# Kernel optimization log

Hardware: AMD Instinct MI355X
Metric: run time of the kernel (lower is better)

## Reference

```python
import jax, jax.numpy as jnp
import numpy as np

B, C, H, W = 2, 64, 192, 192
K = 3
KK = K * K  # 9 kernel taps


def conv2d(x, w, b, dilation=1, padding=1):
    # NCHW / OIHW 3x3 conv, stride 1
    out = jax.lax.conv_general_dilated(
        x, w, window_strides=(1, 1),
        padding=[(padding, padding), (padding, padding)],
        rhs_dilation=(dilation, dilation),
        dimension_numbers=('NCHW', 'OIHW', 'NCHW'))
    return out + b[None, :, None, None]


def channel_ln(x, w, b, eps=1e-5):
    # WithBias_LayerNorm over the channel axis (to_3d puts C last)
    mu = jnp.mean(x, axis=1, keepdims=True)
    var = jnp.mean((x - mu) ** 2, axis=1, keepdims=True)  # biased var
    xn = (x - mu) / jnp.sqrt(var + eps)
    return xn * w[None, :, None, None] + b[None, :, None, None]


def mod_deform_conv(x, offset, mask, w, b):
    # Modulated deformable conv (mmcv semantics): stride 1, pad 1, dil 1,
    # deform_groups=1. offset: [B,2*KK,H,W] (dy,dx interleaved per tap),
    # mask: [B,KK,H,W].
    Bb, Cc, Hh, Ww = x.shape
    off = offset.reshape(Bb, KK, 2, Hh, Ww)
    kidx = jnp.arange(K)
    ky, kx = jnp.meshgrid(kidx, kidx, indexing='ij')
    ky = ky.reshape(KK).astype(x.dtype)
    kx = kx.reshape(KK).astype(x.dtype)
    hh = jnp.arange(Hh, dtype=x.dtype)
    ww = jnp.arange(Ww, dtype=x.dtype)
    # sample positions: out_pos - pad + tap + learned offset  -> [B,KK,H,W]
    py = off[:, :, 0] + hh[None, None, :, None] - 1.0 + ky[None, :, None, None]
    px = off[:, :, 1] + ww[None, None, None, :] - 1.0 + kx[None, :, None, None]
    y0f = jnp.floor(py)
    x0f = jnp.floor(px)
    ly = py - y0f
    lx = px - x0f
    y0 = y0f.astype(jnp.int32)
    x0 = x0f.astype(jnp.int32)
    xf = x.reshape(Bb, Cc, Hh * Ww)

    def corner(yi, xi, wgt):
        valid = (yi >= 0) & (yi < Hh) & (xi >= 0) & (xi < Ww)
        idx = (jnp.clip(yi, 0, Hh - 1) * Ww + jnp.clip(xi, 0, Ww - 1)).reshape(Bb, -1)
        g = jax.vmap(lambda xb, ib: xb[:, ib])(xf, idx)  # [B,C,KK*H*W]
        wv = (wgt * valid.astype(x.dtype)).reshape(Bb, 1, -1)
        return g * wv

    val = (corner(y0, x0, (1 - ly) * (1 - lx))
           + corner(y0, x0 + 1, (1 - ly) * lx)
           + corner(y0 + 1, x0, ly * (1 - lx))
           + corner(y0 + 1, x0 + 1, ly * lx))
    val = val.reshape(Bb, Cc, KK, Hh, Ww) * mask[:, None]  # modulate
    out = jnp.einsum('bckhw,ock->bohw', val, w.reshape(w.shape[0], Cc, KK))
    return out + b[None, :, None, None]


def setup_inputs() -> dict:
    key = jax.random.key(0)
    ks = jax.random.split(key, 8)
    x = jax.random.normal(ks[0], (B, C, H, W), jnp.float32)
    pre_mask = jax.random.uniform(ks[1], (B, 1, H, W), jnp.float32)
    ln_w = jnp.ones((C,), jnp.float32)
    ln_b = jnp.zeros((C,), jnp.float32)
    # offset/mask convs are zero-init in the original; use small random
    # weights so the bilinear gather is actually exercised (offsets ~ few px)
    off_w = jax.random.normal(ks[2], (2 * KK, C, 3, 3), jnp.float32) * 0.02
    off_b = jnp.zeros((2 * KK,), jnp.float32)
    mask_w = jax.random.normal(ks[3], (KK, C, 3, 3), jnp.float32) * 0.02
    mask_b = jnp.zeros((KK,), jnp.float32)
    scale = 1.0 / np.sqrt(C * KK)
    def_w = jax.random.normal(ks[4], (C, C, 3, 3), jnp.float32) * scale
    def_b = jnp.zeros((C,), jnp.float32)
    fus_w = jax.random.normal(ks[5], (C, C, 3, 3), jnp.float32) * scale
    fus_b = jnp.zeros((C,), jnp.float32)
    return {'x': x, 'pre_mask': pre_mask, 'ln_w': ln_w, 'ln_b': ln_b,
            'off_w': off_w, 'off_b': off_b, 'mask_w': mask_w, 'mask_b': mask_b,
            'def_w': def_w, 'def_b': def_b, 'fus_w': fus_w, 'fus_b': fus_b}


def reference(x, pre_mask, ln_w, ln_b, off_w, off_b, mask_w, mask_b,
              def_w, def_b, fus_w, fus_b):
    inp = x
    xn = channel_ln(x, ln_w, ln_b)
    # only the dilation=1 offset/mask branch feeds the single def_conv
    offset = conv2d(xn, off_w, off_b, dilation=1, padding=1)
    mask = jax.nn.sigmoid(conv2d(xn, mask_w, mask_b, dilation=1, padding=1))
    x_def = mod_deform_conv(xn, offset, mask, def_w, def_b)
    # single def_conv -> stack+sum is identity
    return conv2d(x_def, fus_w, fus_b) * pre_mask + inp * (1.0 - pre_mask)
```

## Files before the change

### kernel.cpp

```cpp
#include <hip/hip_runtime.h>
#include <hip/hip_bf16.h>
#include <math.h>

#define B_ 2
#define C_ 64
#define H_ 192
#define W_ 192
#define HW_ (H_*W_)
#define BHW_ (B_*HW_)
#define KK_ 9
#define CK_ (C_*KK_)
#define KSTEPS_ (CK_/32)
#define TX_ 12
#define WROWS_ 8
#define WCOLS_ 21
#define WCHUNKS_ (WROWS_*WCOLS_*8)
#define FWROWS_ 6
#define FWCOLS_ 18
#define FWCHUNKS_ (FWROWS_*FWCOLS_*8)

typedef __bf16 bf16x8 __attribute__((ext_vector_type(8)));
typedef float  f32x4  __attribute__((ext_vector_type(4)));
typedef unsigned short ushortx8 __attribute__((ext_vector_type(8)));
typedef unsigned short ushortx4 __attribute__((ext_vector_type(4)));

__device__ __forceinline__ float bf2f(unsigned short u) {
    unsigned int t = ((unsigned int)u) << 16;
    return __builtin_bit_cast(float, t);
}
__device__ __forceinline__ unsigned short f2bf(float f) {
    __hip_bfloat16 hb = __float2bfloat16(f);
    return *reinterpret_cast<unsigned short*>(&hb);
}

__global__ void ln_kernel(const float* __restrict__ x,
                          const float* __restrict__ lnw,
                          const float* __restrict__ lnb,
                          unsigned short* __restrict__ xnb) {
    int p = blockIdx.x * blockDim.x + threadIdx.x;
    if (p >= BHW_) return;
    int b = p / HW_, pix = p % HW_;
    const float* xb = x + (size_t)b * C_ * HW_ + pix;
    float v[C_];
    float s = 0.f, s2 = 0.f;
    #pragma unroll
    for (int c = 0; c < C_; ++c) {
        v[c] = xb[(size_t)c * HW_];
        s += v[c]; s2 += v[c] * v[c];
    }
    float mu  = s * (1.0f / C_);
    float var = s2 * (1.0f / C_) - mu * mu;
    float inv = rsqrtf(var + 1e-5f);
    unsigned short* zb = xnb + (size_t)p * 64;
    #pragma unroll
    for (int g = 0; g < 8; ++g) {
        ushortx8 st;
        #pragma unroll
        for (int j = 0; j < 8; ++j) {
            int c = g * 8 + j;
            st[j] = f2bf((v[c] - mu) * inv * lnw[c] + lnb[c]);
        }
        *reinterpret_cast<ushortx8*>(zb + g * 8) = st;
    }
}

__global__ void prepack_kernel(const float* __restrict__ dw,
                               const float* __restrict__ fw,
                               const float* __restrict__ offw,
                               const float* __restrict__ maskw,
                               unsigned short* __restrict__ wpack,
                               unsigned short* __restrict__ wpf,
                               unsigned short* __restrict__ wpc) {
    const int n1 = 4 * KSTEPS_ * 64 * 8;
    const int n2 = 4 * KSTEPS_ * 64 * 8;
    const int n3 = 2 * KSTEPS_ * 64 * 8;
    int gid = blockIdx.x * blockDim.x + threadIdx.x;
    int nth = gridDim.x * blockDim.x;
    for (int idx = gid; idx < n1 + n2 + n3; idx += nth) {
        int which = (idx < n1) ? 0 : (idx < n1 + n2 ? 1 : 2);
        int rem = idx - (which == 0 ? 0 : (which == 1 ? n1 : n1 + n2));
        int j = rem & 7;
        int l = (rem >> 3) & 63;
        int rest = rem >> 9;
        int s = rest % KSTEPS_;
        int t = rest / KSTEPS_;
        int oc = t * 16 + (l & 15);
        int ck = s * 32 + (l >> 4) * 8 + j;
        int k = ck >> 6, c = ck & 63;
        float v;
        if (which == 0) {
            v = dw[(size_t)oc * CK_ + c * 9 + k];
        } else if (which == 1) {
            v = fw[(size_t)oc * CK_ + c * 9 + k];
        } else {
            v = (oc < 18) ? offw[(size_t)oc * CK_ + c * 9 + k]
              : (oc < 27) ? maskw[(size_t)(oc - 18) * CK_ + c * 9 + k]
              : 0.f;
        }
        unsigned short u = f2bf(v);
        if (which == 0) wpack[rem] = u;
        else if (which == 1) wpf[rem] = u;
        else wpc[rem] = u;
    }
}

__global__ void __launch_bounds__(128) dc_mfma(
        const unsigned short* __restrict__ xnb,
        const unsigned short* __restrict__ wpc,
        const float* __restrict__ offb, const float* __restrict__ maskb,
        const unsigned short* __restrict__ wpack,
        const float* __restrict__ db,
        unsigned short* __restrict__ xdefb) {
    __shared__ ushortx8 win[WCHUNKS_];
    __shared__ float som[2][32][36];
    int tid  = threadIdx.x;
    int wave = tid >> 6;
    int lane = tid & 63;
    int bid  = blockIdx.x;
    int rg   = bid % (H_ / 4);
    int rest = bid / (H_ / 4);
    int tx   = rest % TX_;
    int b    = rest / TX_;
    int pq = lane & 15;
    int kchunk = lane >> 4;
    int h0 = rg * 4;
    int w0 = tx * 16, w = w0 + pq;
    int hh0 = h0 + 2 * wave, hh1 = hh0 + 1;

    const unsigned short* xb = xnb + (size_t)b * HW_ * 64;

    #pragma unroll
    for (int i = 0; i < 11; ++i) {
        int idx = i * 128 + tid;
        if (idx < WCHUNKS_) {
            int r    = idx / (WCOLS_ * 8);
            int rem2 = idx - r * (WCOLS_ * 8);
            int c    = rem2 >> 3;
            int seg  = rem2 & 7;
            int gy = min(max(h0 - 2 + r, 0), H_ - 1);
            int gx = min(max(w0 - 2 + c, 0), W_ - 1);
            ushortx8 v = *reinterpret_cast<const ushortx8*>(
                xb + ((size_t)(gy * W_ + gx) * 64 + seg * 8));
            win[(r * WCOLS_ + c) * 8 + (seg ^ (c & 7))] = v;
        }
    }
    __syncthreads();

    f32x4 cacc[2][2];
    #pragma unroll
    for (int pg = 0; pg < 2; ++pg)
        #pragma unroll
        for (int t = 0; t < 2; ++t) cacc[pg][t] = f32x4{0.f, 0.f, 0.f, 0.f};

    #pragma unroll
    for (int s = 0; s < KSTEPS_; ++s) {
        const int k = s >> 1;
        const int dy = k / 3 - 1, dxk = k % 3 - 1;
        int wc = pq + dxk + 2;
        int sidx = ((s & 1) * 4 + kchunk) ^ (wc & 7);
        bf16x8 bv[2];
        #pragma unroll
        for (int pg = 0; pg < 2; ++pg) {
            int hp = (pg ? hh1 : hh0);
            bool ok = ((unsigned)(hp + dy) < (unsigned)H_) &&
                      ((unsigned)(w + dxk) < (unsigned)W_);
            int wr = 2 * wave + pg + dy + 2;
            ushortx8 u = win[(wr * WCOLS_ + wc) * 8 + sidx];
            if (!ok) u = ushortx8{0, 0, 0, 0, 0, 0, 0, 0};
            bv[pg] = __builtin_bit_cast(bf16x8, u);
        }
        #pragma unroll
        for (int t = 0; t < 2; ++t) {
            bf16x8 afrag = *reinterpret_cast<const bf16x8*>(
                wpc + ((size_t)(t * KSTEPS_ + s) * 64 + lane) * 8);
            cacc[0][t] = __builtin_amdgcn_mfma_f32_16x16x32_bf16(afrag, bv[0], cacc[0][t], 0, 0, 0);
            cacc[1][t] = __builtin_amdgcn_mfma_f32_16x16x32_bf16(afrag, bv[1], cacc[1][t], 0, 0, 0);
        }
    }

    #pragma unroll
    for (int pg = 0; pg < 2; ++pg) {
        #pragma unroll
        for (int t = 0; t < 2; ++t) {
            f32x4 sv;
            #pragma unroll
            for (int r = 0; r < 4; ++r) {
                int oc = t * 16 + kchunk * 4 + r;
                float a = cacc[pg][t][r];
                if (oc < 18)      sv[r] = a + offb[oc];
                else if (oc < 27) sv[r] = 1.f / (1.f + expf(-(a + maskb[oc - 18])));
                else              sv[r] = 0.f;
            }
            *reinterpret_cast<f32x4*>(&som[wave][pg * 16 + pq][t * 16 + kchunk * 4]) = sv;
        }
    }

    const float* omA = som[wave][pq];
    const float* omB = som[wave][16 + pq];

    f32x4 acc[2][4];
    #pragma unroll
    for (int pg = 0; pg < 2; ++pg)
        #pragma unroll
        for (int t = 0; t < 4; ++t) acc[pg][t] = f32x4{0.f, 0.f, 0.f, 0.f};

    #pragma unroll
    for (int k = 0; k < KK_; ++k) {
        float qA[4], qB[4];
        int cbA[4], sxA[4], cbB[4], sxB[4];
        bool inA[4], inB[4];
        int gaA[4], gaB[4];
        #pragma unroll
        for (int pg = 0; pg < 2; ++pg) {
            const float* om = pg ? omB : omA;
            int hp = pg ? hh1 : hh0;
            float dy = om[2 * k], dx = om[2 * k + 1], m = om[18 + k];
            float py = dy + (float)(hp - 1 + k / 3);
            float px = dx + (float)(w - 1 + k % 3);
            float fy = floorf(py), fx = floorf(px);
            float ly = py - fy, lx = px - fx;
            int y0 = (int)fy, x0 = (int)fx;
            int y1 = y0 + 1, x1 = x0 + 1;
            bool oky0 = (unsigned)y0 < (unsigned)H_;
            bool oky1 = (unsigned)y1 < (unsigned)H_;
            bool okx0 = (unsigned)x0 < (unsigned)W_;
            bool okx1 = (unsigned)x1 < (unsigned)W_;
            float* q = pg ? qB : qA;
            q[0] = (oky0 && okx0) ? (1.f - ly) * (1.f - lx) * m : 0.f;
            q[1] = (oky0 && okx1) ? (1.f - ly) * lx * m : 0.f;
            q[2] = (oky1 && okx0) ? ly * (1.f - lx) * m : 0.f;
            q[3] = (oky1 && okx1) ? ly * lx * m : 0.f;
            int wr0 = y0 - (h0 - 2), wr1 = y1 - (h0 - 2);
            int wc0 = x0 - (w0 - 2), wc1 = x1 - (w0 - 2);
            bool inr0 = (unsigned)wr0 < (unsigned)WROWS_;
            bool inr1 = (unsigned)wr1 < (unsigned)WROWS_;
            bool inc0 = (unsigned)wc0 < (unsigned)WCOLS_;
            bool inc1 = (unsigned)wc1 < (unsigned)WCOLS_;
            bool* in = pg ? inB : inA;
            in[0] = inr0 && inc0; in[1] = inr0 && inc1;
            in[2] = inr1 && inc0; in[3] = inr1 && inc1;
            int swr0 = min(max(wr0, 0), WROWS_ - 1), swr1 = min(max(wr1, 0), WROWS_ - 1);
            int swc0 = min(max(wc0, 0), WCOLS_ - 1), swc1 = min(max(wc1, 0), WCOLS_ - 1);
            int* cb = pg ? cbB : cbA;
            int* sx = pg ? sxB : sxA;
            cb[0] = (swr0 * WCOLS_ + swc0) * 8; sx[0] = swc0 & 7;
            cb[1] = (swr0 * WCOLS_ + swc1) * 8; sx[1] = swc1 & 7;
            cb[2] = (swr1 * WCOLS_ + swc0) * 8; sx[2] = swc0 & 7;
            cb[3] = (swr1 * WCOLS_ + swc1) * 8; sx[3] = swc1 & 7;
            int cy0 = min(max(y0, 0), H_ - 1), cy1 = min(max(y1, 0), H_ - 1);
            int cx0 = min(max(x0, 0), W_ - 1), cx1 = min(max(x1, 0), W_ - 1);
            int* ga = pg ? gaB : gaA;
            ga[0] = cy0 * W_ + cx0; ga[1] = cy0 * W_ + cx1;
            ga[2] = cy1 * W_ + cx0; ga[3] = cy1 * W_ + cx1;
        }

        #pragma unroll
        for (int half = 0; half < 2; ++half) {
            int s = k * 2 + half;
            int seg = half * 4 + kchunk;
            int cbg = half * 32 + kchunk * 8;
            bf16x8 af[4];
            #pragma unroll
            for (int t = 0; t < 4; ++t)
                af[t] = *reinterpret_cast<const bf16x8*>(
                    wpack + ((size_t)(t * KSTEPS_ + s) * 64 + lane) * 8);
            ushortx8 vA[4], vB[4];
            #pragma unroll
            for (int c = 0; c < 4; ++c) vA[c] = win[cbA[c] + (seg ^ sxA[c])];
            #pragma unroll
            for (int c = 0; c < 4; ++c) vB[c] = win[cbB[c] + (seg ^ sxB[c])];
            #pragma unroll
            for (int c = 0; c < 4; ++c) {
                if (qA[c] != 0.f && !inA[c])
                    vA[c] = *reinterpret_cast<const ushortx8*>(xb + ((size_t)gaA[c] * 64 + cbg));
                if (qB[c] != 0.f && !inB[c])
                    vB[c] = *reinterpret_cast<const ushortx8*>(xb + ((size_t)gaB[c] * 64 + cbg));
            }
            union { unsigned short u[8]; bf16x8 v; } buA, buB;
            #pragma unroll
            for (int j = 0; j < 8; ++j) {
                float a = qA[0] * bf2f(vA[0][j]) + qA[1] * bf2f(vA[1][j])
                        + qA[2] * bf2f(vA[2][j]) + qA[3] * bf2f(vA[3][j]);
                buA.u[j] = f2bf(a);
                float bvv = qB[0] * bf2f(vB[0][j]) + qB[1] * bf2f(vB[1][j])
                          + qB[2] * bf2f(vB[2][j]) + qB[3] * bf2f(vB[3][j]);
                buB.u[j] = f2bf(bvv);
            }
            #pragma unroll
            for (int t = 0; t < 4; ++t) {
                acc[0][t] = __builtin_amdgcn_mfma_f32_16x16x32_bf16(af[t], buA.v, acc[0][t], 0, 0, 0);
                acc[1][t] = __builtin_amdgcn_mfma_f32_16x16x32_bf16(af[t], buB.v, acc[1][t], 0, 0, 0);
            }
        }
    }

    #pragma unroll
    for (int pg = 0; pg < 2; ++pg) {
        int hp = pg ? hh1 : hh0;
        unsigned short* zb = xdefb + ((size_t)(b * HW_ + hp * W_ + w)) * 64;
        #pragma unroll
        for (int t = 0; t < 4; ++t) {
            ushortx4 st;
            #pragma unroll
            for (int r = 0; r < 4; ++r) {
                int oc = t * 16 + kchunk * 4 + r;
                st[r] = f2bf(acc[pg][t][r] + db[oc]);
            }
            *reinterpret_cast<ushortx4*>(zb + t * 16 + kchunk * 4) = st;
        }
    }
}

__global__ void __launch_bounds__(128) fuse_mfma(
        const unsigned short* __restrict__ xdefb,
        const unsigned short* __restrict__ wpf,
        const float* __restrict__ fb,
        const float* __restrict__ premask,
        const float* __restrict__ xin,
        float* __restrict__ out) {
    __shared__ ushortx8 fwin[FWCHUNKS_];
    int tid  = threadIdx.x;
    int wave = tid >> 6;
    int lane = tid & 63;
    int bid  = blockIdx.x;
    int rg   = bid % (H_ / 4);
    int rest = bid / (H_ / 4);
    int tx   = rest % TX_;
    int b    = rest / TX_;
    int pq = lane & 15;
    int kchunk = lane >> 4;
    int h0 = rg * 4;
    int w0 = tx * 16, w = w0 + pq;
    int hh0 = h0 + 2 * wave, hh1 = hh0 + 1;

    const unsigned short* xb = xdefb + (size_t)b * HW_ * 64;

    #pragma unroll
    for (int i = 0; i < 7; ++i) {
        int idx = i * 128 + tid;
        if (idx < FWCHUNKS_) {
            int r    = idx / (FWCOLS_ * 8);
            int rem2 = idx - r * (FWCOLS_ * 8);
            int c    = rem2 >> 3;
            int seg  = rem2 & 7;
            int gy = min(max(h0 - 1 + r, 0), H_ - 1);
            int gx = min(max(w0 - 1 + c, 0), W_ - 1);
            ushortx8 v = *reinterpret_cast<const ushortx8*>(
                xb + ((size_t)(gy * W_ + gx) * 64 + seg * 8));
            fwin[(r * FWCOLS_ + c) * 8 + (seg ^ (c & 7))] = v;
        }
    }
    __syncthreads();

    f32x4 acc[2][4];
    #pragma unroll
    for (int pg = 0; pg < 2; ++pg)
        #pragma unroll
        for (int t = 0; t < 4; ++t) acc[pg][t] = f32x4{0.f, 0.f, 0.f, 0.f};

    #pragma unroll
    for (int s = 0; s < KSTEPS_; ++s) {
        const int k = s >> 1;
        const int dy = k / 3 - 1, dxk = k % 3 - 1;
        int wc = pq + dxk + 1;
        int sidx = ((s & 1) * 4 + kchunk) ^ (wc & 7);
        bf16x8 bv[2];
        #pragma unroll
        for (int pg = 0; pg < 2; ++pg) {
            int hp = (pg ? hh1 : hh0);
            bool ok = ((unsigned)(hp + dy) < (unsigned)H_) &&
                      ((unsigned)(w + dxk) < (unsigned)W_);
            int wr = 2 * wave + pg + dy + 1;
            ushortx8 u = fwin[(wr * FWCOLS_ + wc) * 8 + sidx];
            if (!ok) u = ushortx8{0, 0, 0, 0, 0, 0, 0, 0};
            bv[pg] = __builtin_bit_cast(bf16x8, u);
        }
        #pragma unroll
        for (int t = 0; t < 4; ++t) {
            bf16x8 afrag = *reinterpret_cast<const bf16x8*>(
                wpf + ((size_t)(t * KSTEPS_ + s) * 64 + lane) * 8);
            acc[0][t] = __builtin_amdgcn_mfma_f32_16x16x32_bf16(afrag, bv[0], acc[0][t], 0, 0, 0);
            acc[1][t] = __builtin_amdgcn_mfma_f32_16x16x32_bf16(afrag, bv[1], acc[1][t], 0, 0, 0);
        }
    }

    #pragma unroll
    for (int pg = 0; pg < 2; ++pg) {
        int hp = pg ? hh1 : hh0;
        int pix = hp * W_ + w;
        float pm = premask[(size_t)b * HW_ + pix];
        #pragma unroll
        for (int t = 0; t < 4; ++t) {
            #pragma unroll
            for (int r = 0; r < 4; ++r) {
                int oc = t * 16 + kchunk * 4 + r;
                size_t oidx = ((size_t)b * C_ + oc) * HW_ + pix;
                out[oidx] = (acc[pg][t][r] + fb[oc]) * pm + xin[oidx] * (1.f - pm);
            }
        }
    }
}

extern "C" void kernel_launch(void* const* d_in, const int* in_sizes, int n_in,
                              void* d_out, int out_size, void* d_ws, size_t ws_size,
                              hipStream_t stream) {
    const float* x       = (const float*)d_in[0];
    const float* premask = (const float*)d_in[1];
    const float* lnw     = (const float*)d_in[2];
    const float* lnb     = (const float*)d_in[3];
    const float* offw    = (const float*)d_in[4];
    const float* offb    = (const float*)d_in[5];
    const float* maskw   = (const float*)d_in[6];
    const float* maskb   = (const float*)d_in[7];
    const float* dw      = (const float*)d_in[8];
    const float* db      = (const float*)d_in[9];
    const float* fw      = (const float*)d_in[10];
    const float* fb      = (const float*)d_in[11];
    float* out = (float*)d_out;

    char* ws = (char*)d_ws;
    unsigned short* xnb   = (unsigned short*)ws;  ws += sizeof(short) * (size_t)BHW_ * 64;
    unsigned short* xdefb = (unsigned short*)ws;  ws += sizeof(short) * (size_t)BHW_ * 64;
    unsigned short* wpack = (unsigned short*)ws;  ws += sizeof(short) * 4 * KSTEPS_ * 64 * 8;
    unsigned short* wpf   = (unsigned short*)ws;  ws += sizeof(short) * 4 * KSTEPS_ * 64 * 8;
    unsigned short* wpc   = (unsigned short*)ws;  ws += sizeof(short) * 2 * KSTEPS_ * 64 * 8;

    const int grid = B_ * TX_ * (H_ / 4);

    ln_kernel<<<(BHW_ + 255) / 256, 256, 0, stream>>>(x, lnw, lnb, xnb);
    prepack_kernel<<<36, 256, 0, stream>>>(dw, fw, offw, maskw, wpack, wpf, wpc);
    dc_mfma<<<grid, 128, 0, stream>>>(
        xnb, wpc, offb, maskb, wpack, db, xdefb);
    fuse_mfma<<<grid, 128, 0, stream>>>(xdefb, wpf, fb, premask, x, out);
}
```

Before: 79.00 us.

## Process four rows per wave and merge LayerNorm with weight prepacking

Each block now covers 8 output rows instead of 4, so each wave handles 4 rows. Loaded weight fragments are reused across four pixel groups, and the halo overhead of the shared-memory window shrinks relative to the tile. The LayerNorm and weight-prepack kernels are merged into one launch that selects its work by block index, removing one launch. The trade-off is a larger accumulator register footprint and half as many blocks (576), which may lower occupancy and fill the GPU less evenly.

After: 94.25 us. 19.3% more time.

```diff
diff --git a/kernel.cpp b/kernel.cpp
--- a/kernel.cpp
+++ b/kernel.cpp
@@ -12,10 +12,11 @@
 #define CK_ (C_*KK_)
 #define KSTEPS_ (CK_/32)
 #define TX_ 12
-#define WROWS_ 8
+#define RB_ 8
+#define WROWS_ 12
 #define WCOLS_ 21
 #define WCHUNKS_ (WROWS_*WCOLS_*8)
-#define FWROWS_ 6
+#define FWROWS_ 10
 #define FWCOLS_ 18
 #define FWCHUNKS_ (FWROWS_*FWCOLS_*8)
 
@@ -33,49 +34,49 @@
     return *reinterpret_cast<unsigned short*>(&hb);
 }
 
-__global__ void ln_kernel(const float* __restrict__ x,
-                          const float* __restrict__ lnw,
-                          const float* __restrict__ lnb,
-                          unsigned short* __restrict__ xnb) {
-    int p = blockIdx.x * blockDim.x + threadIdx.x;
-    if (p >= BHW_) return;
-    int b = p / HW_, pix = p % HW_;
-    const float* xb = x + (size_t)b * C_ * HW_ + pix;
-    float v[C_];
-    float s = 0.f, s2 = 0.f;
-    #pragma unroll
-    for (int c = 0; c < C_; ++c) {
-        v[c] = xb[(size_t)c * HW_];
-        s += v[c]; s2 += v[c] * v[c];
-    }
-    float mu  = s * (1.0f / C_);
-    float var = s2 * (1.0f / C_) - mu * mu;
-    float inv = rsqrtf(var + 1e-5f);
-    unsigned short* zb = xnb + (size_t)p * 64;
-    #pragma unroll
-    for (int g = 0; g < 8; ++g) {
-        ushortx8 st;
-        #pragma unroll
-        for (int j = 0; j < 8; ++j) {
-            int c = g * 8 + j;
-            st[j] = f2bf((v[c] - mu) * inv * lnw[c] + lnb[c]);
-        }
-        *reinterpret_cast<ushortx8*>(zb + g * 8) = st;
-    }
-}
-
-__global__ void prepack_kernel(const float* __restrict__ dw,
-                               const float* __restrict__ fw,
-                               const float* __restrict__ offw,
-                               const float* __restrict__ maskw,
-                               unsigned short* __restrict__ wpack,
-                               unsigned short* __restrict__ wpf,
-                               unsigned short* __restrict__ wpc) {
+__global__ void ln_prepack_kernel(const float* __restrict__ x,
+                                  const float* __restrict__ lnw,
+                                  const float* __restrict__ lnb,
+                                  unsigned short* __restrict__ xnb,
+                                  const float* __restrict__ dw,
+                                  const float* __restrict__ fw,
+                                  const float* __restrict__ offw,
+                                  const float* __restrict__ maskw,
+                                  unsigned short* __restrict__ wpack,
+                                  unsigned short* __restrict__ wpf,
+                                  unsigned short* __restrict__ wpc) {
+    if (blockIdx.x < 288) {
+        int p = blockIdx.x * 256 + threadIdx.x;
+        int b = p / HW_, pix = p % HW_;
+        const float* xb = x + (size_t)b * C_ * HW_ + pix;
+        float v[C_];
+        float s = 0.f, s2 = 0.f;
+        #pragma unroll
+        for (int c = 0; c < C_; ++c) {
+            v[c] = xb[(size_t)c * HW_];
+            s += v[c]; s2 += v[c] * v[c];
+        }
+        float mu  = s * (1.0f / C_);
+        float var = s2 * (1.0f / C_) - mu * mu;
+        float inv = rsqrtf(var + 1e-5f);
+        unsigned short* zb = xnb + (size_t)p * 64;
+        #pragma unroll
+        for (int g = 0; g < 8; ++g) {
+            ushortx8 st;
+            #pragma unroll
+            for (int j = 0; j < 8; ++j) {
+                int c = g * 8 + j;
+                st[j] = f2bf((v[c] - mu) * inv * lnw[c] + lnb[c]);
+            }
+            *reinterpret_cast<ushortx8*>(zb + g * 8) = st;
+        }
+        return;
+    }
     const int n1 = 4 * KSTEPS_ * 64 * 8;
     const int n2 = 4 * KSTEPS_ * 64 * 8;
     const int n3 = 2 * KSTEPS_ * 64 * 8;
-    int gid = blockIdx.x * blockDim.x + threadIdx.x;
-    int nth = gridDim.x * blockDim.x;
+    int gid = (blockIdx.x - 288) * 256 + threadIdx.x;
+    int nth = 36 * 256;
     for (int idx = gid; idx < n1 + n2 + n3; idx += nth) {
         int which = (idx < n1) ? 0 : (idx < n1 + n2 ? 1 : 2);
         int rem = idx - (which == 0 ? 0 : (which == 1 ? n1 : n1 + n2));
@@ -112,25 +113,25 @@
         const float* __restrict__ db,
         unsigned short* __restrict__ xdefb) {
     __shared__ ushortx8 win[WCHUNKS_];
-    __shared__ float som[2][32][36];
+    __shared__ float som[2][64][36];
     int tid  = threadIdx.x;
     int wave = tid >> 6;
     int lane = tid & 63;
     int bid  = blockIdx.x;
-    int rg   = bid % (H_ / 4);
-    int rest = bid / (H_ / 4);
+    int rg   = bid % (H_ / RB_);
+    int rest = bid / (H_ / RB_);
     int tx   = rest % TX_;
     int b    = rest / TX_;
     int pq = lane & 15;
     int kchunk = lane >> 4;
-    int h0 = rg * 4;
+    int h0 = rg * RB_;
     int w0 = tx * 16, w = w0 + pq;
-    int hh0 = h0 + 2 * wave, hh1 = hh0 + 1;
+    int hbase = h0 + 4 * wave;
 
     const unsigned short* xb = xnb + (size_t)b * HW_ * 64;
 
     #pragma unroll
-    for (int i = 0; i < 11; ++i) {
+    for (int i = 0; i < 16; ++i) {
         int idx = i * 128 + tid;
         if (idx < WCHUNKS_) {
             int r    = idx / (WCOLS_ * 8);
@@ -146,9 +147,9 @@
     }
     __syncthreads();
 
-    f32x4 cacc[2][2];
-    #pragma unroll
-    for (int pg = 0; pg < 2; ++pg)
+    f32x4 cacc[4][2];
+    #pragma unroll
+    for (int pg = 0; pg < 4; ++pg)
         #pragma unroll
         for (int t = 0; t < 2; ++t) cacc[pg][t] = f32x4{0.f, 0.f, 0.f, 0.f};
 
@@ -158,28 +159,28 @@
         const int dy = k / 3 - 1, dxk = k % 3 - 1;
         int wc = pq + dxk + 2;
         int sidx = ((s & 1) * 4 + kchunk) ^ (wc & 7);
-        bf16x8 bv[2];
-        #pragma unroll
-        for (int pg = 0; pg < 2; ++pg) {
-            int hp = (pg ? hh1 : hh0);
+        bf16x8 af[2];
+        #pragma unroll
+        for (int t = 0; t < 2; ++t)
+            af[t] = *reinterpret_cast<const bf16x8*>(
+                wpc + ((size_t)(t * KSTEPS_ + s) * 64 + lane) * 8);
+        #pragma unroll
+        for (int pg = 0; pg < 4; ++pg) {
+            int hp = hbase + pg;
             bool ok = ((unsigned)(hp + dy) < (unsigned)H_) &&
                       ((unsigned)(w + dxk) < (unsigned)W_);
-            int wr = 2 * wave + pg + dy + 2;
+            int wr = 4 * wave + pg + dy + 2;
             ushortx8 u = win[(wr * WCOLS_ + wc) * 8 + sidx];
             if (!ok) u = ushortx8{0, 0, 0, 0, 0, 0, 0, 0};
-            bv[pg] = __builtin_bit_cast(bf16x8, u);
-        }
-        #pragma unroll
-        for (int t = 0; t < 2; ++t) {
-            bf16x8 afrag = *reinterpret_cast<const bf16x8*>(
-                wpc + ((size_t)(t * KSTEPS_ + s) * 64 + lane) * 8);
-            cacc[0][t] = __builtin_amdgcn_mfma_f32_16x16x32_bf16(afrag, bv[0], cacc[0][t], 0, 0, 0);
-            cacc[1][t] = __builtin_amdgcn_mfma_f32_16x16x32_bf16(afrag, bv[1], cacc[1][t], 0, 0, 0);
-        }
-    }
-
-    #pragma unroll
-    for (int pg = 0; pg < 2; ++pg) {
+            bf16x8 bv = __builtin_bit_cast(bf16x8, u);
+            #pragma unroll
+            for (int t = 0; t < 2; ++t)
+                cacc[pg][t] = __builtin_amdgcn_mfma_f32_16x16x32_bf16(af[t], bv, cacc[pg][t], 0, 0, 0);
+        }
+    }
+
+    #pragma unroll
+    for (int pg = 0; pg < 4; ++pg) {
         #pragma unroll
         for (int t = 0; t < 2; ++t) {
             f32x4 sv;
@@ -195,25 +196,26 @@
         }
     }
 
-    const float* omA = som[wave][pq];
-    const float* omB = som[wave][16 + pq];
-
-    f32x4 acc[2][4];
-    #pragma unroll
-    for (int pg = 0; pg < 2; ++pg)
+    f32x4 acc[4][4];
+    #pragma unroll
+    for (int pg = 0; pg < 4; ++pg)
         #pragma unroll
         for (int t = 0; t < 4; ++t) acc[pg][t] = f32x4{0.f, 0.f, 0.f, 0.f};
 
     #pragma unroll
     for (int k = 0; k < KK_; ++k) {
-        float qA[4], qB[4];
-        int cbA[4], sxA[4], cbB[4], sxB[4];
-        bool inA[4], inB[4];
-        int gaA[4], gaB[4];
-        #pragma unroll
-        for (int pg = 0; pg < 2; ++pg) {
-            const float* om = pg ? omB : omA;
-            int hp = pg ? hh1 : hh0;
+        bf16x8 af[2][4];
+        #pragma unroll
+        for (int half = 0; half < 2; ++half)
+            #pragma unroll
+            for (int t = 0; t < 4; ++t)
+                af[half][t] = *reinterpret_cast<const bf16x8*>(
+                    wpack + ((size_t)(t * KSTEPS_ + (k * 2 + half)) * 64 + lane) * 8);
+
+        #pragma unroll
+        for (int pg = 0; pg < 4; ++pg) {
+            int hp = hbase + pg;
+            const float* om = som[wave][pg * 16 + pq];
             float dy = om[2 * k], dx = om[2 * k + 1], m = om[18 + k];
             float py = dy + (float)(hp - 1 + k / 3);
             float px = dx + (float)(w - 1 + k % 3);
@@ -225,7 +227,7 @@
             bool oky1 = (unsigned)y1 < (unsigned)H_;
             bool okx0 = (unsigned)x0 < (unsigned)W_;
             bool okx1 = (unsigned)x1 < (unsigned)W_;
-            float* q = pg ? qB : qA;
+            float q[4];
             q[0] = (oky0 && okx0) ? (1.f - ly) * (1.f - lx) * m : 0.f;
             q[1] = (oky0 && okx1) ? (1.f - ly) * lx * m : 0.f;
             q[2] = (oky1 && okx0) ? ly * (1.f - lx) * m : 0.f;
@@ -236,67 +238,52 @@
             bool inr1 = (unsigned)wr1 < (unsigned)WROWS_;
             bool inc0 = (unsigned)wc0 < (unsigned)WCOLS_;
             bool inc1 = (unsigned)wc1 < (unsigned)WCOLS_;
-            bool* in = pg ? inB : inA;
+            bool in[4];
             in[0] = inr0 && inc0; in[1] = inr0 && inc1;
             in[2] = inr1 && inc0; in[3] = inr1 && inc1;
             int swr0 = min(max(wr0, 0), WROWS_ - 1), swr1 = min(max(wr1, 0), WROWS_ - 1);
             int swc0 = min(max(wc0, 0), WCOLS_ - 1), swc1 = min(max(wc1, 0), WCOLS_ - 1);
-            int* cb = pg ? cbB : cbA;
-            int* sx = pg ? sxB : sxA;
+            int cb[4], sx[4];
             cb[0] = (swr0 * WCOLS_ + swc0) * 8; sx[0] = swc0 & 7;
             cb[1] = (swr0 * WCOLS_ + swc1) * 8; sx[1] = swc1 & 7;
             cb[2] = (swr1 * WCOLS_ + swc0) * 8; sx[2] = swc0 & 7;
             cb[3] = (swr1 * WCOLS_ + swc1) * 8; sx[3] = swc1 & 7;
             int cy0 = min(max(y0, 0), H_ - 1), cy1 = min(max(y1, 0), H_ - 1);
             int cx0 = min(max(x0, 0), W_ - 1), cx1 = min(max(x1, 0), W_ - 1);
-            int* ga = pg ? gaB : gaA;
+            int ga[4];
             ga[0] = cy0 * W_ + cx0; ga[1] = cy0 * W_ + cx1;
             ga[2] = cy1 * W_ + cx0; ga[3] = cy1 * W_ + cx1;
-        }
-
-        #pragma unroll
-        for (int half = 0; half < 2; ++half) {
-            int s = k * 2 + half;
-            int seg = half * 4 + kchunk;
-            int cbg = half * 32 + kchunk * 8;
-            bf16x8 af[4];
-            #pragma unroll
-            for (int t = 0; t < 4; ++t)
-                af[t] = *reinterpret_cast<const bf16x8*>(
-                    wpack + ((size_t)(t * KSTEPS_ + s) * 64 + lane) * 8);
-            ushortx8 vA[4], vB[4];
-            #pragma unroll
-            for (int c = 0; c < 4; ++c) vA[c] = win[cbA[c] + (seg ^ sxA[c])];
-            #pragma unroll
-            for (int c = 0; c < 4; ++c) vB[c] = win[cbB[c] + (seg ^ sxB[c])];
-            #pragma unroll
-            for (int c = 0; c < 4; ++c) {
-                if (qA[c] != 0.f && !inA[c])
-                    vA[c] = *reinterpret_cast<const ushortx8*>(xb + ((size_t)gaA[c] * 64 + cbg));
-                if (qB[c] != 0.f && !inB[c])
-                    vB[c] = *reinterpret_cast<const ushortx8*>(xb + ((size_t)gaB[c] * 64 + cbg));
+
+            #pragma unroll
+            for (int half = 0; half < 2; ++half) {
+                int seg = half * 4 + kchunk;
+                int cbg = half * 32 + kchunk * 8;
+                ushortx8 v[4];
+                #pragma unroll
+                for (int c = 0; c < 4; ++c) v[c] = win[cb[c] + (seg ^ sx[c])];
+                #pragma unroll
+                for (int c = 0; c < 4; ++c)
+                    if (q[c] != 0.f && !in[c])
+                        v[c] = *reinterpret_cast<const ushortx8*>(
+                            xb + ((size_t)ga[c] * 64 + cbg));
+                union { unsigned short u[8]; bf16x8 v; } bu;
+                #pragma unroll
+                for (int j = 0; j < 8; ++j) {
+                    float a = q[0] * bf2f(v[0][j]) + q[1] * bf2f(v[1][j])
+                            + q[2] * bf2f(v[2][j]) + q[3] * bf2f(v[3][j]);
+                    bu.u[j] = f2bf(a);
+                }
+                #pragma unroll
+                for (int t = 0; t < 4; ++t)
+                    acc[pg][t] = __builtin_amdgcn_mfma_f32_16x16x32_bf16(
+                        af[half][t], bu.v, acc[pg][t], 0, 0, 0);
             }
-            union { unsigned short u[8]; bf16x8 v; } buA, buB;
-            #pragma unroll
-            for (int j = 0; j < 8; ++j) {
-                float a = qA[0] * bf2f(vA[0][j]) + qA[1] * bf2f(vA[1][j])
-                        + qA[2] * bf2f(vA[2][j]) + qA[3] * bf2f(vA[3][j]);
-                buA.u[j] = f2bf(a);
-                float bvv = qB[0] * bf2f(vB[0][j]) + qB[1] * bf2f(vB[1][j])
-                          + qB[2] * bf2f(vB[2][j]) + qB[3] * bf2f(vB[3][j]);
-                buB.u[j] = f2bf(bvv);
-            }
-            #pragma unroll
-            for (int t = 0; t < 4; ++t) {
-                acc[0][t] = __builtin_amdgcn_mfma_f32_16x16x32_bf16(af[t], buA.v, acc[0][t], 0, 0, 0);
-                acc[1][t] = __builtin_amdgcn_mfma_f32_16x16x32_bf16(af[t], buB.v, acc[1][t], 0, 0, 0);
-            }
-        }
-    }
-
-    #pragma unroll
-    for (int pg = 0; pg < 2; ++pg) {
-        int hp = pg ? hh1 : hh0;
+        }
+    }
+
+    #pragma unroll
+    for (int pg = 0; pg < 4; ++pg) {
+        int hp = hbase + pg;
         unsigned short* zb = xdefb + ((size_t)(b * HW_ + hp * W_ + w)) * 64;
         #pragma unroll
         for (int t = 0; t < 4; ++t) {
@@ -323,20 +310,20 @@
     int wave = tid >> 6;
     int lane = tid & 63;
     int bid  = blockIdx.x;
-    int rg   = bid % (H_ / 4);
-    int rest = bid / (H_ / 4);
+    int rg   = bid % (H_ / RB_);
+    int rest = bid / (H_ / RB_);
     int tx   = rest % TX_;
     int b    = rest / TX_;
     int pq = lane & 15;
     int kchunk = lane >> 4;
-    int h0 = rg * 4;
+    int h0 = rg * RB_;
     int w0 = tx * 16, w = w0 + pq;
-    int hh0 = h0 + 2 * wave, hh1 = hh0 + 1;
+    int hbase = h0 + 4 * wave;
 
     const unsigned short* xb = xdefb + (size_t)b * HW_ * 64;
 
     #pragma unroll
-    for (int i = 0; i < 7; ++i) {
+    for (int i = 0; i < 12; ++i) {
         int idx = i * 128 + tid;
         if (idx < FWCHUNKS_) {
             int r    = idx / (FWCOLS_ * 8);
@@ -352,9 +339,9 @@
     }
     __syncthreads();
 
-    f32x4 acc[2][4];
-    #pragma unroll
-    for (int pg = 0; pg < 2; ++pg)
+    f32x4 acc[4][4];
+    #pragma unroll
+    for (int pg = 0; pg < 4; ++pg)
         #pragma unroll
         for (int t = 0; t < 4; ++t) acc[pg][t] = f32x4{0.f, 0.f, 0.f, 0.f};
 
@@ -364,29 +351,29 @@
         const int dy = k / 3 - 1, dxk = k % 3 - 1;
         int wc = pq + dxk + 1;
         int sidx = ((s & 1) * 4 + kchunk) ^ (wc & 7);
-        bf16x8 bv[2];
-        #pragma unroll
-        for (int pg = 0; pg < 2; ++pg) {
-            int hp = (pg ? hh1 : hh0);
+        bf16x8 af[4];
+        #pragma unroll
+        for (int t = 0; t < 4; ++t)
+            af[t] = *reinterpret_cast<const bf16x8*>(
+                wpf + ((size_t)(t * KSTEPS_ + s) * 64 + lane) * 8);
+        #pragma unroll
+        for (int pg = 0; pg < 4; ++pg) {
+            int hp = hbase + pg;
             bool ok = ((unsigned)(hp + dy) < (unsigned)H_) &&
                       ((unsigned)(w + dxk) < (unsigned)W_);
-            int wr = 2 * wave + pg + dy + 1;
+            int wr = 4 * wave + pg + dy + 1;
             ushortx8 u = fwin[(wr * FWCOLS_ + wc) * 8 + sidx];
             if (!ok) u = ushortx8{0, 0, 0, 0, 0, 0, 0, 0};
-            bv[pg] = __builtin_bit_cast(bf16x8, u);
-        }
-        #pragma unroll
-        for (int t = 0; t < 4; ++t) {
-            bf16x8 afrag = *reinterpret_cast<const bf16x8*>(
-                wpf + ((size_t)(t * KSTEPS_ + s) * 64 + lane) * 8);
-            acc[0][t] = __builtin_amdgcn_mfma_f32_16x16x32_bf16(afrag, bv[0], acc[0][t], 0, 0, 0);
-            acc[1][t] = __builtin_amdgcn_mfma_f32_16x16x32_bf16(afrag, bv[1], acc[1][t], 0, 0, 0);
-        }
-    }
-
-    #pragma unroll
-    for (int pg = 0; pg < 2; ++pg) {
-        int hp = pg ? hh1 : hh0;
+            bf16x8 bv = __builtin_bit_cast(bf16x8, u);
+            #pragma unroll
+            for (int t = 0; t < 4; ++t)
+                acc[pg][t] = __builtin_amdgcn_mfma_f32_16x16x32_bf16(af[t], bv, acc[pg][t], 0, 0, 0);
+        }
+    }
+
+    #pragma unroll
+    for (int pg = 0; pg < 4; ++pg) {
+        int hp = hbase + pg;
         int pix = hp * W_ + w;
         float pm = premask[(size_t)b * HW_ + pix];
         #pragma unroll
@@ -425,10 +412,10 @@
     unsigned short* wpf   = (unsigned short*)ws;  ws += sizeof(short) * 4 * KSTEPS_ * 64 * 8;
     unsigned short* wpc   = (unsigned short*)ws;  ws += sizeof(short) * 2 * KSTEPS_ * 64 * 8;
 
-    const int grid = B_ * TX_ * (H_ / 4);
-
-    ln_kernel<<<(BHW_ + 255) / 256, 256, 0, stream>>>(x, lnw, lnb, xnb);
-    prepack_kernel<<<36, 256, 0, stream>>>(dw, fw, offw, maskw, wpack, wpf, wpc);
+    const int grid = B_ * TX_ * (H_ / RB_);
+
+    ln_prepack_kernel<<<288 + 36, 256, 0, stream>>>(
+        x, lnw, lnb, xnb, dw, fw, offw, maskw, wpack, wpf, wpc);
     dc_mfma<<<grid, 128, 0, stream>>>(
         xnb, wpc, offb, maskb, wpack, db, xdefb);
     fuse_mfma<<<grid, 128, 0, stream>>>(xdefb, wpf, fb, premask, x, out);
```
